# Kernel optimization log

Measured on AMD Instinct MI355X. Metric: run time of the kernel, lower is better.

## Reference

```python
import jax, jax.numpy as jnp
import numpy as np

TOKENS, D_IN, D_OUT, RANK = 32768, 1024, 1024, 16
SCALE1 = 8.0 / RANK   # alpha=8, rank=16
SCALE2 = 16.0 / RANK  # alpha=16, rank=16


def setup_inputs() -> dict:
    key = jax.random.key(0)
    ks = jax.random.split(key, 7)
    inv = 1.0 / np.sqrt(D_IN)
    return {
        "x": jax.random.normal(ks[0], (TOKENS, D_IN), jnp.float32),
        "W": jax.random.normal(ks[1], (D_OUT, D_IN), jnp.float32) * inv,
        "b": jax.random.normal(ks[2], (D_OUT,), jnp.float32) * 0.01,
        "A1": jax.random.normal(ks[3], (RANK, D_IN), jnp.float32) * inv,
        "B1": jax.random.normal(ks[4], (D_OUT, RANK), jnp.float32) * 0.01,
        "A2": jax.random.normal(ks[5], (RANK, D_IN), jnp.float32) * inv,
        "B2": jax.random.normal(ks[6], (D_OUT, RANK), jnp.float32) * 0.01,
    }


def reference(x, W, b, A1, B1, A2, B2):
    # base linear: [T, D_in] @ [D_in, D_out] + b
    out = jnp.einsum("ti,oi->to", x, W) + b
    # LoRA adapter 1: scale * (x @ A1^T) @ B1^T   (dropout=Identity in eval)
    out = out + SCALE1 * jnp.einsum("tr,or->to", jnp.einsum("ti,ri->tr", x, A1), B1)
    # LoRA adapter 2
    out = out + SCALE2 * jnp.einsum("tr,or->to", jnp.einsum("ti,ri->tr", x, A2), B2)
    return out
```

## Files before the change

### kernel.cpp

```cpp
#include <hip/hip_runtime.h>

#define TOKENS 32768
#define DIN 1024
#define DOUT 1024
#define RANK 16
#define SCALE1 0.5f
#define SCALE2 1.0f

#define BM 128
#define BN 128
#define BK 32

typedef __bf16 bf16x8 __attribute__((ext_vector_type(8)));
typedef float f32x4 __attribute__((ext_vector_type(4)));

__device__ __forceinline__ void load_lds16(const void* gptr, void* lptr) {
    __builtin_amdgcn_global_load_lds(
        (__attribute__((address_space(1))) void*)gptr,
        (__attribute__((address_space(3))) void*)lptr, 16, 0, 0);
}

__global__ void weff_kernel(const float* __restrict__ W, const float* __restrict__ A1,
                            const float* __restrict__ B1, const float* __restrict__ A2,
                            const float* __restrict__ B2, __bf16* __restrict__ Weff) {
    int idx = blockIdx.x * blockDim.x + threadIdx.x;
    int o = idx >> 10;
    int i = idx & 1023;
    float s1 = 0.f, s2 = 0.f;
#pragma unroll
    for (int r = 0; r < RANK; ++r) {
        s1 += B1[o * RANK + r] * A1[r * DIN + i];
        s2 += B2[o * RANK + r] * A2[r * DIN + i];
    }
    Weff[idx] = (__bf16)(W[idx] + SCALE1 * s1 + SCALE2 * s2);
}

__global__ void cvt_x_kernel(const float* __restrict__ x, __bf16* __restrict__ xb) {
    int i = (blockIdx.x * blockDim.x + threadIdx.x) * 8;
    float4 a = *(const float4*)(x + i);
    float4 b = *(const float4*)(x + i + 4);
    bf16x8 v;
    v[0] = (__bf16)a.x; v[1] = (__bf16)a.y; v[2] = (__bf16)a.z; v[3] = (__bf16)a.w;
    v[4] = (__bf16)b.x; v[5] = (__bf16)b.y; v[6] = (__bf16)b.z; v[7] = (__bf16)b.w;
    *(bf16x8*)(xb + i) = v;
}

__global__ __launch_bounds__(256) void gemm_bt_kernel(
    const __bf16* __restrict__ A,
    const __bf16* __restrict__ Bw,
    const float* __restrict__ bias, float* __restrict__ C) {
    __shared__ alignas(16) __bf16 lsA[2][BM * BK];
    __shared__ alignas(16) __bf16 lsB[2][BN * BK];

    const int tid = threadIdx.x;
    const int wave = tid >> 6;
    const int lane = tid & 63;
    const int m0 = blockIdx.y * BM;
    const int n0 = blockIdx.x * BN;
    const int wm = wave >> 1;
    const int wn = wave & 1;

    const int lrow = lane >> 2;
    const int lcol = ((lane & 3) ^ ((lane >> 3) & 3)) * 8;

    const __bf16* gA = A + (size_t)(m0 + wave * 32 + lrow) * DIN + lcol;
    const __bf16* gB = Bw + (size_t)(n0 + wave * 32 + lrow) * DIN + lcol;
    const int so0 = (wave * 32) * BK;
    const int so1 = (wave * 32 + 16) * BK;

    f32x4 acc[4][4];
#pragma unroll
    for (int i = 0; i < 4; ++i)
#pragma unroll
        for (int j = 0; j < 4; ++j) acc[i][j] = f32x4{0.f, 0.f, 0.f, 0.f};

    const int fr = lane & 15;
    const int fsw = ((lane >> 4) ^ ((lane >> 1) & 3)) * 8;

    load_lds16(gA, &lsA[0][so0]);
    load_lds16(gA + 16 * DIN, &lsA[0][so1]);
    load_lds16(gB, &lsB[0][so0]);
    load_lds16(gB + 16 * DIN, &lsB[0][so1]);

    int cur = 0;
    for (int k0 = 0; k0 < DIN; k0 += BK) {
        __syncthreads();

        if (k0 + BK < DIN) {
            const int kn = k0 + BK;
            load_lds16(gA + kn, &lsA[cur ^ 1][so0]);
            load_lds16(gA + kn + 16 * DIN, &lsA[cur ^ 1][so1]);
            load_lds16(gB + kn, &lsB[cur ^ 1][so0]);
            load_lds16(gB + kn + 16 * DIN, &lsB[cur ^ 1][so1]);
        }

        bf16x8 af[4], bfv[4];
#pragma unroll
        for (int t = 0; t < 4; ++t) {
            af[t] = *(const bf16x8*)&lsA[cur][(wm * 64 + t * 16 + fr) * BK + fsw];
            bfv[t] = *(const bf16x8*)&lsB[cur][(wn * 64 + t * 16 + fr) * BK + fsw];
        }
#pragma unroll
        for (int mt = 0; mt < 4; ++mt)
#pragma unroll
            for (int nt = 0; nt < 4; ++nt)
                acc[mt][nt] = __builtin_amdgcn_mfma_f32_16x16x32_bf16(
                    af[mt], bfv[nt], acc[mt][nt], 0, 0, 0);
        cur ^= 1;
    }

    const int rbase = (lane >> 4) * 4;
#pragma unroll
    for (int nt = 0; nt < 4; ++nt) {
        const int n = n0 + wn * 64 + nt * 16 + fr;
        const float bv = bias[n];
#pragma unroll
        for (int mt = 0; mt < 4; ++mt) {
            const int m = m0 + wm * 64 + mt * 16 + rbase;
            float* cp = C + (size_t)m * DOUT + n;
#pragma unroll
            for (int r = 0; r < 4; ++r) cp[(size_t)r * DOUT] = acc[mt][nt][r] + bv;
        }
    }
}

extern "C" void kernel_launch(void* const* d_in, const int* in_sizes, int n_in,
                              void* d_out, int out_size, void* d_ws, size_t ws_size,
                              hipStream_t stream) {
    const float* x  = (const float*)d_in[0];
    const float* W  = (const float*)d_in[1];
    const float* b  = (const float*)d_in[2];
    const float* A1 = (const float*)d_in[3];
    const float* B1 = (const float*)d_in[4];
    const float* A2 = (const float*)d_in[5];
    const float* B2 = (const float*)d_in[6];
    float* out = (float*)d_out;

    __bf16* xb   = (__bf16*)d_ws;
    __bf16* Weff = (__bf16*)((char*)d_ws + (size_t)TOKENS * DIN * sizeof(__bf16));

    cvt_x_kernel<<<TOKENS * DIN / (256 * 8), 256, 0, stream>>>(x, xb);
    weff_kernel<<<DOUT * DIN / 256, 256, 0, stream>>>(W, A1, B1, A2, B2, Weff);
    gemm_bt_kernel<<<dim3(DOUT / BN, TOKENS / BM), 256, 0, stream>>>(xb, Weff, b, out);
}
```

Measured before the change: 341.6 us.

## Fuse fp32-to-bf16 conversion of x into GEMM A-tile loads, remap blocks per XCD

Removes the separate cvt_x kernel and its bf16 workspace copy. The GEMM now loads fp32 x tiles into registers, converts them to bf16 and writes them into swizzled LDS, with the next tile's loads issued before the MFMA loop and the stores placed after it. This avoids a full extra read and write of x through HBM. The 2D grid also becomes 1D with an XCD-aware mapping, so each XCD gets contiguous M rows and covers all N tiles, to improve L2 reuse of x. The cost is doubled global read bytes for A inside the GEMM, plus more registers and VALU conversion work.

```diff
diff --git a/kernel.cpp b/kernel.cpp
--- a/kernel.cpp
+++ b/kernel.cpp
@@ -20,6 +20,13 @@
         (__attribute__((address_space(3))) void*)lptr, 16, 0, 0);
 }
 
+__device__ __forceinline__ void store_cvt(__bf16* dst, float4 a, float4 b) {
+    bf16x8 v;
+    v[0] = (__bf16)a.x; v[1] = (__bf16)a.y; v[2] = (__bf16)a.z; v[3] = (__bf16)a.w;
+    v[4] = (__bf16)b.x; v[5] = (__bf16)b.y; v[6] = (__bf16)b.z; v[7] = (__bf16)b.w;
+    *(bf16x8*)dst = v;
+}
+
 __global__ void weff_kernel(const float* __restrict__ W, const float* __restrict__ A1,
                             const float* __restrict__ B1, const float* __restrict__ A2,
                             const float* __restrict__ B2, __bf16* __restrict__ Weff) {
@@ -35,18 +42,8 @@
     Weff[idx] = (__bf16)(W[idx] + SCALE1 * s1 + SCALE2 * s2);
 }
 
-__global__ void cvt_x_kernel(const float* __restrict__ x, __bf16* __restrict__ xb) {
-    int i = (blockIdx.x * blockDim.x + threadIdx.x) * 8;
-    float4 a = *(const float4*)(x + i);
-    float4 b = *(const float4*)(x + i + 4);
-    bf16x8 v;
-    v[0] = (__bf16)a.x; v[1] = (__bf16)a.y; v[2] = (__bf16)a.z; v[3] = (__bf16)a.w;
-    v[4] = (__bf16)b.x; v[5] = (__bf16)b.y; v[6] = (__bf16)b.z; v[7] = (__bf16)b.w;
-    *(bf16x8*)(xb + i) = v;
-}
-
 __global__ __launch_bounds__(256) void gemm_bt_kernel(
-    const __bf16* __restrict__ A,
+    const float* __restrict__ X,
     const __bf16* __restrict__ Bw,
     const float* __restrict__ bias, float* __restrict__ C) {
     __shared__ alignas(16) __bf16 lsA[2][BM * BK];
@@ -55,18 +52,26 @@
     const int tid = threadIdx.x;
     const int wave = tid >> 6;
     const int lane = tid & 63;
-    const int m0 = blockIdx.y * BM;
-    const int n0 = blockIdx.x * BN;
+
+    const int l = blockIdx.x;
+    const int xcd = l & 7;
+    const int s = l >> 3;
+    const int m0 = (xcd * 32 + (s >> 3)) * BM;
+    const int n0 = (s & 7) * BN;
+
     const int wm = wave >> 1;
     const int wn = wave & 1;
 
+    const int arow = tid >> 2;
+    const int ach = tid & 3;
+    const float* pA = X + (size_t)(m0 + arow) * DIN + ach * 8;
+    const int aoff = arow * BK + (ach ^ ((arow >> 1) & 3)) * 8;
+
     const int lrow = lane >> 2;
     const int lcol = ((lane & 3) ^ ((lane >> 3) & 3)) * 8;
-
-    const __bf16* gA = A + (size_t)(m0 + wave * 32 + lrow) * DIN + lcol;
     const __bf16* gB = Bw + (size_t)(n0 + wave * 32 + lrow) * DIN + lcol;
     const int so0 = (wave * 32) * BK;
-    const int so1 = (wave * 32 + 16) * BK;
+    const int so1 = so0 + 16 * BK;
 
     f32x4 acc[4][4];
 #pragma unroll
@@ -77,21 +82,30 @@
     const int fr = lane & 15;
     const int fsw = ((lane >> 4) ^ ((lane >> 1) & 3)) * 8;
 
-    load_lds16(gA, &lsA[0][so0]);
-    load_lds16(gA + 16 * DIN, &lsA[0][so1]);
-    load_lds16(gB, &lsB[0][so0]);
-    load_lds16(gB + 16 * DIN, &lsB[0][so1]);
+    {
+        float4 u0 = *(const float4*)(pA);
+        float4 v0 = *(const float4*)(pA + 4);
+        float4 u1 = *(const float4*)(pA + (size_t)64 * DIN);
+        float4 v1 = *(const float4*)(pA + (size_t)64 * DIN + 4);
+        store_cvt(&lsA[0][aoff], u0, v0);
+        store_cvt(&lsA[0][aoff + 64 * BK], u1, v1);
+        load_lds16(gB, &lsB[0][so0]);
+        load_lds16(gB + 16 * DIN, &lsB[0][so1]);
+    }
+    __syncthreads();
 
     int cur = 0;
     for (int k0 = 0; k0 < DIN; k0 += BK) {
-        __syncthreads();
-
-        if (k0 + BK < DIN) {
-            const int kn = k0 + BK;
-            load_lds16(gA + kn, &lsA[cur ^ 1][so0]);
-            load_lds16(gA + kn + 16 * DIN, &lsA[cur ^ 1][so1]);
-            load_lds16(gB + kn, &lsB[cur ^ 1][so0]);
-            load_lds16(gB + kn + 16 * DIN, &lsB[cur ^ 1][so1]);
+        const bool more = (k0 + BK) < DIN;
+        float4 u0, v0, u1, v1;
+        if (more) {
+            const float* p = pA + k0 + BK;
+            u0 = *(const float4*)(p);
+            v0 = *(const float4*)(p + 4);
+            u1 = *(const float4*)(p + (size_t)64 * DIN);
+            v1 = *(const float4*)(p + (size_t)64 * DIN + 4);
+            load_lds16(gB + k0 + BK, &lsB[cur ^ 1][so0]);
+            load_lds16(gB + k0 + BK + 16 * DIN, &lsB[cur ^ 1][so1]);
         }
 
         bf16x8 af[4], bfv[4];
@@ -106,6 +120,12 @@
             for (int nt = 0; nt < 4; ++nt)
                 acc[mt][nt] = __builtin_amdgcn_mfma_f32_16x16x32_bf16(
                     af[mt], bfv[nt], acc[mt][nt], 0, 0, 0);
+
+        if (more) {
+            store_cvt(&lsA[cur ^ 1][aoff], u0, v0);
+            store_cvt(&lsA[cur ^ 1][aoff + 64 * BK], u1, v1);
+            __syncthreads();
+        }
         cur ^= 1;
     }
 
@@ -136,10 +156,8 @@
     const float* B2 = (const float*)d_in[6];
     float* out = (float*)d_out;
 
-    __bf16* xb   = (__bf16*)d_ws;
-    __bf16* Weff = (__bf16*)((char*)d_ws + (size_t)TOKENS * DIN * sizeof(__bf16));
+    __bf16* Weff = (__bf16*)d_ws;
 
-    cvt_x_kernel<<<TOKENS * DIN / (256 * 8), 256, 0, stream>>>(x, xb);
     weff_kernel<<<DOUT * DIN / 256, 256, 0, stream>>>(W, A1, B1, A2, B2, Weff);
-    gemm_bt_kernel<<<dim3(DOUT / BN, TOKENS / BM), 256, 0, stream>>>(xb, Weff, b, out);
+    gemm_bt_kernel<<<(TOKENS / BM) * (DOUT / BN), 256, 0, stream>>>(x, Weff, b, out);
 }
```

Measured after the change: 422.5 us. 23.7% more time.
